# Optimization experiments

Measured on AMD Instinct MI355X. Metric: run time of the kernel, lower is better.

Reference implementation:

```python
import jax, jax.numpy as jnp
import numpy as np

B, C, H, W = 32, 3, 512, 512

def setup_inputs() -> dict:
    key = jax.random.key(0)
    k1, k2 = jax.random.split(key)
    # pixel values in [0, 255], matching the byte-image assumption of the module
    prediction = jax.random.uniform(k1, (B, C, H, W), dtype=jnp.float32) * 255.0
    target = jax.random.uniform(k2, (B, C, H, W), dtype=jnp.float32) * 255.0
    return {"prediction": prediction, "target": target}

def _v_channel(x):
    # Faithful to: clamp(x*1, 0, 255).byte() -> cv2 RGB2HSV -> V channel.
    # For uint8 images, OpenCV's V channel is exactly max(R, G, B); the byte
    # cast truncates fractional parts, reproduced here with floor.
    q = jnp.floor(jnp.clip(x, 0.0, 255.0))  # [B,3,H,W] quantized to integers
    return jnp.max(q, axis=1)  # [B,H,W] value channel = max over RGB

def reference(prediction, target):
    v_pred = _v_channel(prediction)   # [B,H,W]
    v_tgt = _v_channel(target)        # [B,H,W]
    # torch.min/max over dim=1 of [B,H,W] reduces the height axis -> [B,W]
    dark_loss = jnp.mean((jnp.min(v_pred, axis=1) - jnp.min(v_tgt, axis=1)) ** 2)
    bright_loss = jnp.mean((jnp.max(v_pred, axis=1) - jnp.max(v_tgt, axis=1)) ** 2)
    return dark_loss + bright_loss
```

## Files before the change

kernel.cpp:

```cpp
#include <hip/hip_runtime.h>
#include <cfloat>

#define B_   32
#define H_   512
#define W_   512
#define HW_  (H_ * W_)
#define CHW_ (3 * HW_)
#define W4_  (W_ / 4)
#define HC_  16
#define ROWS_ (H_ / HC_)

__device__ __forceinline__ float max3f(float a, float b, float c) {
    return fmaxf(fmaxf(a, b), c);
}
__device__ __forceinline__ float4 min4(float4 a, float4 b) {
    return make_float4(fminf(a.x, b.x), fminf(a.y, b.y), fminf(a.z, b.z), fminf(a.w, b.w));
}
__device__ __forceinline__ float4 max4(float4 a, float4 b) {
    return make_float4(fmaxf(a.x, b.x), fmaxf(a.y, b.y), fmaxf(a.z, b.z), fmaxf(a.w, b.w));
}
__device__ __forceinline__ float qclip(float m) {
    return floorf(fminf(fmaxf(m, 0.0f), 255.0f));
}

__global__ __launch_bounds__(128) void s1_minmax(
        const float* __restrict__ pred, const float* __restrict__ tgt,
        float* __restrict__ ws) {
    const int inp   = blockIdx.x & 1;
    const int bc    = blockIdx.x >> 1;
    const int b     = bc >> 4;
    const int chunk = bc & (HC_ - 1);
    const int w4    = threadIdx.x;

    const float4* S = reinterpret_cast<const float4*>(inp ? tgt : pred)
                      + (size_t)b * (CHW_ / 4);

    float4 mn = make_float4( FLT_MAX,  FLT_MAX,  FLT_MAX,  FLT_MAX);
    float4 mx = make_float4(-FLT_MAX, -FLT_MAX, -FLT_MAX, -FLT_MAX);

    const int h0 = chunk * ROWS_;
    #pragma unroll 8
    for (int h = h0; h < h0 + ROWS_; ++h) {
        const int base = h * W4_ + w4;
        float4 a  = S[base];
        float4 g  = S[base +      (HW_ / 4)];
        float4 c2 = S[base + 2 * (HW_ / 4)];
        float4 v = make_float4(max3f(a.x, g.x, c2.x), max3f(a.y, g.y, c2.y),
                               max3f(a.z, g.z, c2.z), max3f(a.w, g.w, c2.w));
        mn = min4(mn, v);
        mx = max4(mx, v);
    }

    const size_t arr = (size_t)B_ * HC_ * W4_;
    const size_t o   = ((size_t)b * HC_ + chunk) * W4_ + w4;
    float4* wsv = reinterpret_cast<float4*>(ws);
    wsv[o + (size_t)(2 * inp + 0) * arr] = mn;
    wsv[o + (size_t)(2 * inp + 1) * arr] = mx;
}

__global__ __launch_bounds__(256) void s2a_reduce(
        const float* __restrict__ ws, double* __restrict__ partial) {
    const int i = blockIdx.x * 256 + threadIdx.x;
    const int b = i >> 9;
    const int w = i & (W_ - 1);

    const size_t arr = (size_t)B_ * HC_ * W_;
    const float* minP = ws;
    const float* maxP = ws + arr;
    const float* minT = ws + 2 * arr;
    const float* maxT = ws + 3 * arr;

    float mnP = FLT_MAX, mxP = -FLT_MAX, mnT = FLT_MAX, mxT = -FLT_MAX;
    #pragma unroll 4
    for (int c = 0; c < HC_; ++c) {
        const size_t o = ((size_t)b * HC_ + c) * W_ + w;
        mnP = fminf(mnP, minP[o]);
        mxP = fmaxf(mxP, maxP[o]);
        mnT = fminf(mnT, minT[o]);
        mxT = fmaxf(mxT, maxT[o]);
    }
    const float dmin = qclip(mnP) - qclip(mnT);
    const float dmax = qclip(mxP) - qclip(mxT);
    double s = (double)dmin * (double)dmin + (double)dmax * (double)dmax;

    __shared__ double sd[256];
    sd[threadIdx.x] = s;
    __syncthreads();
    #pragma unroll
    for (int st = 128; st > 0; st >>= 1) {
        if (threadIdx.x < st) sd[threadIdx.x] += sd[threadIdx.x + st];
        __syncthreads();
    }
    if (threadIdx.x == 0) partial[blockIdx.x] = sd[0];
}

__global__ __launch_bounds__(64) void s2b_final(
        const double* __restrict__ partial, float* __restrict__ out) {
    __shared__ double sd[64];
    sd[threadIdx.x] = partial[threadIdx.x];
    __syncthreads();
    #pragma unroll
    for (int st = 32; st > 0; st >>= 1) {
        if (threadIdx.x < st) sd[threadIdx.x] += sd[threadIdx.x + st];
        __syncthreads();
    }
    if (threadIdx.x == 0) out[0] = (float)(sd[0] / (double)(B_ * W_));
}

extern "C" void kernel_launch(void* const* d_in, const int* in_sizes, int n_in,
                              void* d_out, int out_size, void* d_ws, size_t ws_size,
                              hipStream_t stream) {
    const float* pred = (const float*)d_in[0];
    const float* tgt  = (const float*)d_in[1];
    float* out = (float*)d_out;
    float* wsf = (float*)d_ws;
    double* partial = (double*)(wsf + (size_t)4 * B_ * HC_ * W_);

    hipLaunchKernelGGL(s1_minmax, dim3(2 * B_ * HC_), dim3(128), 0, stream,
                       pred, tgt, wsf);
    hipLaunchKernelGGL(s2a_reduce, dim3(64), dim3(256), 0, stream,
                       wsf, partial);
    hipLaunchKernelGGL(s2b_final, dim3(1), dim3(64), 0, stream,
                       partial, out);
}
```

Before: 40.27 us.

## Fuse final reduction into s2 via last-block atomic counter; double stage-1 chunks

Removes the third kernel launch by having the last finishing block of the second-stage reduction, found with an atomic counter, sum the 64 partials with wave shuffles. The counter is reset inside the first kernel. Separately, the number of height chunks is doubled to 32, giving stage 1 twice as many blocks (2048) for more memory-level parallelism, at the cost of twice the workspace traffic in stage 2. The atomic release/acquire ordering adds some synchronisation overhead.

```diff
diff --git a/kernel.cpp b/kernel.cpp
--- a/kernel.cpp
+++ b/kernel.cpp
@@ -7,8 +7,9 @@
 #define HW_  (H_ * W_)
 #define CHW_ (3 * HW_)
 #define W4_  (W_ / 4)
-#define HC_  16
+#define HC_  32
 #define ROWS_ (H_ / HC_)
+#define NP_   64
 
 __device__ __forceinline__ float max3f(float a, float b, float c) {
     return fmaxf(fmaxf(a, b), c);
@@ -25,10 +26,13 @@
 
 __global__ __launch_bounds__(128) void s1_minmax(
         const float* __restrict__ pred, const float* __restrict__ tgt,
-        float* __restrict__ ws) {
+        float* __restrict__ ws, unsigned int* __restrict__ counter) {
+    if (blockIdx.x == 0 && threadIdx.x == 0)
+        __hip_atomic_store(counter, 0u, __ATOMIC_RELAXED, __HIP_MEMORY_SCOPE_AGENT);
+
     const int inp   = blockIdx.x & 1;
     const int bc    = blockIdx.x >> 1;
-    const int b     = bc >> 4;
+    const int b     = bc >> 5;
     const int chunk = bc & (HC_ - 1);
     const int w4    = threadIdx.x;
 
@@ -58,8 +62,9 @@
     wsv[o + (size_t)(2 * inp + 1) * arr] = mx;
 }
 
-__global__ __launch_bounds__(256) void s2a_reduce(
-        const float* __restrict__ ws, double* __restrict__ partial) {
+__global__ __launch_bounds__(256) void s2_reduce(
+        const float* __restrict__ ws, double* __restrict__ partial,
+        unsigned int* __restrict__ counter, float* __restrict__ out) {
     const int i = blockIdx.x * 256 + threadIdx.x;
     const int b = i >> 9;
     const int w = i & (W_ - 1);
@@ -84,6 +89,7 @@
     double s = (double)dmin * (double)dmin + (double)dmax * (double)dmax;
 
     __shared__ double sd[256];
+    __shared__ int lastFlag;
     sd[threadIdx.x] = s;
     __syncthreads();
     #pragma unroll
@@ -91,20 +97,22 @@
         if (threadIdx.x < st) sd[threadIdx.x] += sd[threadIdx.x + st];
         __syncthreads();
     }
-    if (threadIdx.x == 0) partial[blockIdx.x] = sd[0];
-}
+    if (threadIdx.x == 0) {
+        __hip_atomic_store(&partial[blockIdx.x], sd[0],
+                           __ATOMIC_RELEASE, __HIP_MEMORY_SCOPE_AGENT);
+        unsigned int t = __hip_atomic_fetch_add(counter, 1u,
+                           __ATOMIC_ACQ_REL, __HIP_MEMORY_SCOPE_AGENT);
+        lastFlag = (t == NP_ - 1);
+    }
+    __syncthreads();
 
-__global__ __launch_bounds__(64) void s2b_final(
-        const double* __restrict__ partial, float* __restrict__ out) {
-    __shared__ double sd[64];
-    sd[threadIdx.x] = partial[threadIdx.x];
-    __syncthreads();
-    #pragma unroll
-    for (int st = 32; st > 0; st >>= 1) {
-        if (threadIdx.x < st) sd[threadIdx.x] += sd[threadIdx.x + st];
-        __syncthreads();
+    if (lastFlag && threadIdx.x < 64) {
+        double v = __hip_atomic_load(&partial[threadIdx.x],
+                                     __ATOMIC_ACQUIRE, __HIP_MEMORY_SCOPE_AGENT);
+        #pragma unroll
+        for (int st = 32; st > 0; st >>= 1) v += __shfl_down(v, st, 64);
+        if (threadIdx.x == 0) out[0] = (float)(v / (double)(B_ * W_));
     }
-    if (threadIdx.x == 0) out[0] = (float)(sd[0] / (double)(B_ * W_));
 }
 
 extern "C" void kernel_launch(void* const* d_in, const int* in_sizes, int n_in,
@@ -114,12 +122,12 @@
     const float* tgt  = (const float*)d_in[1];
     float* out = (float*)d_out;
     float* wsf = (float*)d_ws;
+
     double* partial = (double*)(wsf + (size_t)4 * B_ * HC_ * W_);
+    unsigned int* counter = (unsigned int*)(partial + NP_);
 
     hipLaunchKernelGGL(s1_minmax, dim3(2 * B_ * HC_), dim3(128), 0, stream,
-                       pred, tgt, wsf);
-    hipLaunchKernelGGL(s2a_reduce, dim3(64), dim3(256), 0, stream,
-                       wsf, partial);
-    hipLaunchKernelGGL(s2b_final, dim3(1), dim3(64), 0, stream,
-                       partial, out);
+                       pred, tgt, wsf, counter);
+    hipLaunchKernelGGL(s2_reduce, dim3(NP_), dim3(256), 0, stream,
+                       wsf, partial, counter, out);
 }
```

Result: slower. 43.23 us (+7.3%).
